# Kernel tuning notes

Hardware: AMD Instinct MI355X
Metric: run time of the kernel (lower is better)

The kernel has to match this reference:

```python
import jax, jax.numpy as jnp
import numpy as np


def _conv(x, w, b, stride=1, pad=0):
    # x: NCHW, w: OIHW (torch layout)
    y = jax.lax.conv_general_dilated(
        x, w, (stride, stride), [(pad, pad), (pad, pad)],
        dimension_numbers=('NCHW', 'OIHW', 'NCHW'))
    return y + b[None, :, None, None]


def _convT(x, w, b):
    # torch ConvTranspose2d(k=4, stride=2, padding=1); w: [Cin, Cout, 4, 4]
    wf = jnp.flip(w, (2, 3)).transpose(1, 0, 2, 3)  # -> OIHW
    y = jax.lax.conv_general_dilated(
        x, wf, (1, 1), [(2, 2), (2, 2)], lhs_dilation=(2, 2),
        dimension_numbers=('NCHW', 'OIHW', 'NCHW'))
    return y + b[None, :, None, None]


def _quantize(z, embed):
    # z: [B,H,W,D], embed: [D,K]  (eval-mode _Quantize: no EMA update)
    f = z.reshape(-1, z.shape[-1])
    dist = (f * f).sum(1, keepdims=True) - 2.0 * (f @ embed) + (embed * embed).sum(0, keepdims=True)
    ind = jnp.argmin(dist, axis=1)
    q = embed.T[ind].reshape(z.shape)
    diff = jnp.mean((jax.lax.stop_gradient(q) - z) ** 2)[None]
    q = z + jax.lax.stop_gradient(q - z)  # straight-through
    return q, diff, ind.reshape(z.shape[:-1])


def setup_inputs() -> dict:
    key = jax.random.key(0)
    ks = jax.random.split(key, 22)
    s = 0.02
    r = lambda k, sh, sc=s: jax.random.normal(k, sh, jnp.float32) * sc
    z = lambda sh: jnp.zeros(sh, jnp.float32)
    return {
        'x': jax.random.normal(ks[0], (16, 3, 256, 256), jnp.float32),
        # encoder_bottom: two stride-2 4x4 convs, 3->128->128 (256->64)
        'wb1': r(ks[1], (128, 3, 4, 4)), 'bb1': z(128),
        'wb2': r(ks[2], (128, 128, 4, 4)), 'bb2': z(128),
        # encoder_top: one stride-2 4x4 conv, 128->128 (64->32)
        'wt1': r(ks[3], (128, 128, 4, 4)), 'bt1': z(128),
        # quantize_conv_t: 1x1, 128->64
        'wqt': r(ks[4], (64, 128, 1, 1)), 'bqt': z(64),
        'embed_t': jax.random.normal(ks[5], (64, 512), jnp.float32),
        # decoder_top: convT 64->64 (32->64)
        'wdt': r(ks[6], (64, 64, 4, 4)), 'bdt': z(64),
        # quantize_conv_b: 1x1, 192->64
        'wqb': r(ks[7], (64, 192, 1, 1)), 'bqb': z(64),
        'embed_b': jax.random.normal(ks[8], (64, 512), jnp.float32),
        # upsample_t: convT 64->64 (32->64)
        'wup': r(ks[9], (64, 64, 4, 4)), 'bup': z(64),
        # decoder_bottom: convT 128->64 (64->128), convT 64->3 (128->256)
        'wd1': r(ks[10], (128, 64, 4, 4)), 'bd1': z(64),
        'wd2': r(ks[11], (64, 3, 4, 4)), 'bd2': z(3),
    }


def reference(x, wb1, bb1, wb2, bb2, wt1, bt1, wqt, bqt, embed_t,
              wdt, bdt, wqb, bqb, embed_b, wup, bup, wd1, bd1, wd2, bd2):
    # ----- encode -----
    enc_b = jax.nn.relu(_conv(x, wb1, bb1, stride=2, pad=1))          # [B,128,128,128]
    enc_b = jax.nn.relu(_conv(enc_b, wb2, bb2, stride=2, pad=1))      # [B,128,64,64]
    enc_t = jax.nn.relu(_conv(enc_b, wt1, bt1, stride=2, pad=1))      # [B,128,32,32]

    qt = _conv(enc_t, wqt, bqt).transpose(0, 2, 3, 1)                 # [B,32,32,64]
    quant_t, diff_t, id_t = _quantize(qt, embed_t)
    quant_t = quant_t.transpose(0, 3, 1, 2)                           # [B,64,32,32]

    dec_t = _convT(quant_t, wdt, bdt)                                 # [B,64,64,64]
    enc_cat = jnp.concatenate([dec_t, enc_b], axis=1)                 # [B,192,64,64]

    qb = _conv(enc_cat, wqb, bqb).transpose(0, 2, 3, 1)               # [B,64,64,64]
    quant_b, diff_b, id_b = _quantize(qb, embed_b)
    quant_b = quant_b.transpose(0, 3, 1, 2)                           # [B,64,64,64]

    loss_commit = diff_t + diff_b                                     # [1]

    # ----- decode -----
    up_t = _convT(quant_t, wup, bup)                                  # [B,64,64,64]
    quant = jnp.concatenate([up_t, quant_b], axis=1)                  # [B,128,64,64]
    h = jax.nn.relu(_convT(quant, wd1, bd1))                          # [B,64,128,128]
    x_hat = _convT(h, wd2, bd2)                                       # [B,3,256,256]

    return x_hat, quant_t, quant_b, loss_commit, id_t, id_b
```

## Files before the change

### kernel.cpp

```cpp
#include <hip/hip_runtime.h>

#define TPB 256

typedef __attribute__((ext_vector_type(4))) float f32x4;
typedef __attribute__((ext_vector_type(8))) short bf16x8;

__global__ void wtrans_kernel(const float* __restrict__ src, float* __restrict__ dst,
                              int CIN, int COUT, int taps, int iohw) {
    int idx = blockIdx.x * TPB + threadIdx.x;
    int tot = CIN * COUT * taps;
    if (idx >= tot) return;
    int co = idx % COUT;
    int ci = (idx / COUT) % CIN;
    int tap = idx / (COUT * CIN);
    float v = iohw ? src[(ci * COUT + co) * taps + tap]
                   : src[(co * CIN + ci) * taps + tap];
    dst[idx] = v;
}

__device__ __forceinline__ unsigned bf16_rne(float v) {
    unsigned u = __float_as_uint(v);
    return (u + 0x7FFFu + ((u >> 16) & 1u)) >> 16;
}

__global__ void wtrans_bf16_kernel(const float* __restrict__ src, short* __restrict__ dst,
                                   int CIN, int COUT, int taps, int iohw, int PL) {
    int idx = blockIdx.x * TPB + threadIdx.x;
    int tot = CIN * COUT * taps;
    if (idx >= tot) return;
    int ci = idx % CIN;
    int co = (idx / CIN) % COUT;
    int tap = idx / (CIN * COUT);
    float v = iohw ? src[(ci * COUT + co) * taps + tap]
                   : src[(co * CIN + ci) * taps + tap];
    unsigned h = bf16_rne(v);
    float rem = v - __uint_as_float(h << 16);
    unsigned l = bf16_rne(rem);
    dst[idx] = (short)h;
    dst[idx + PL] = (short)l;
}

__global__ void wtrans_wd2_kernel(const float* __restrict__ src, short* __restrict__ dst) {
    int idx = blockIdx.x * TPB + threadIdx.x;
    if (idx >= 16384) return;
    int ci  = idx & 63;
    int co  = (idx >> 6) & 15;
    int tap = (idx >> 10) & 3;
    int cls = idx >> 12;
    int py = cls >> 1, px = cls & 1;
    int jj = tap >> 1, ii = tap & 1;
    int ky = (1 - py) + 2 * jj;
    int kx = (1 - px) + 2 * ii;
    float v = (co < 3) ? src[(ci * 3 + co) * 16 + ky * 4 + kx] : 0.f;
    dst[idx] = (short)bf16_rne(v);
}

__global__ void etrans_kernel(const float* __restrict__ et, const float* __restrict__ eb,
                              short* __restrict__ ETt, short* __restrict__ ETb) {
    int idx = blockIdx.x * TPB + threadIdx.x;
    if (idx >= 65536) return;
    const float* src = (idx < 32768) ? et : eb;
    short* dst = (idx < 32768) ? ETt : ETb;
    int i = idx & 32767;
    int k = i & 63;
    int n = i >> 6;
    float v = src[k * 512 + n];
    unsigned h = bf16_rne(v);
    float rem = v - __uint_as_float(h << 16);
    dst[i] = (short)h;
    dst[i + 32768] = (short)bf16_rne(rem);
}

__device__ __forceinline__ void cvt_split2(float a, float b, unsigned& hw, unsigned& lw) {
    unsigned ha = bf16_rne(a), hb = bf16_rne(b);
    float ra = a - __uint_as_float(ha << 16);
    float rb = b - __uint_as_float(hb << 16);
    hw = ha | (hb << 16);
    lw = bf16_rne(ra) | (bf16_rne(rb) << 16);
}
__device__ __forceinline__ unsigned cvt_pk(float a, float b) {
    return bf16_rne(a) | (bf16_rne(b) << 16);
}

template<int MODE, int CIN, int COUT, int SPLIT, int RELU,
         int IH, int IW, int OH, int OW, int R>
__global__ __launch_bounds__(256) void mfma_conv(
    const float* __restrict__ in, const short* __restrict__ Wb,
    const float* __restrict__ bias, float* __restrict__ outp) {
    constexpr int TAPS = (MODE == 0) ? 16 : 4;
    constexpr int CW = (MODE == 0) ? OW : OW / 2;
    constexpr int CH = (MODE == 0) ? OH : OH / 2;
    constexpr int NCH = CIN / 32;
    constexpr int MTc = (COUT == 128) ? 4 : 2;
    constexpr long PL = (long)TAPS * COUT * CIN;

    __shared__ short Ah[128 * 40];
    __shared__ short Al[SPLIT ? 128 * 40 : 8];
    __shared__ short Bh[COUT * 40];
    __shared__ short Bl[SPLIT ? COUT * 40 : 8];

    int bx = blockIdx.x;
    int ry = 0, rx = 0;
    if (MODE == 1) { int c = bx & 3; ry = c >> 1; rx = c & 1; bx >>= 2; }
    const int y0 = (bx % (CH / R)) * R;
    const int n  = bx / (CH / R);

    const int tid = threadIdx.x;
    const int p  = tid >> 1;
    const int ak = (tid & 1) * 16;
    const int rr = p / CW, xx = p % CW;
    constexpr int BPT = (COUT * 32) / 256;
    constexpr int TPRB = 32 / BPT;
    const int bco = tid / TPRB;
    const int bk  = (tid % TPRB) * BPT;
    const int lane = tid & 63, wv = tid >> 6;
    const int quad = lane >> 4, l16 = lane & 15;
    const int mbase = (COUT == 128) ? (wv & 1) * 64 : wv * 32;
    const int nbase = (COUT == 128) ? (wv >> 1) * 64 : 0;

    f32x4 acc[MTc][4];
#pragma unroll
    for (int mt = 0; mt < MTc; ++mt)
#pragma unroll
        for (int nt = 0; nt < 4; ++nt) acc[mt][nt] = f32x4{0.f, 0.f, 0.f, 0.f};

#pragma unroll 1
    for (int tap = 0; tap < TAPS; ++tap) {
        int iy, ix, wt;
        if (MODE == 0) {
            int ky = tap >> 2, kx = tap & 3;
            iy = 2 * (y0 + rr) - 1 + ky;
            ix = 2 * xx - 1 + kx;
            wt = tap;
        } else {
            int jj = tap >> 1, ii = tap & 1;
            iy = (y0 + rr) + ry - jj;
            ix = xx + rx - ii;
            wt = ((1 - ry) + 2 * jj) * 4 + ((1 - rx) + 2 * ii);
        }
        const bool av = (iy >= 0) && (iy < IH) && (ix >= 0) && (ix < IW);
        const long abase = ((long)(n * IH + iy) * IW + ix) * CIN + ak;
        const short* wrh = Wb + ((long)wt * COUT + bco) * CIN + bk;

#pragma unroll 1
        for (int cb = 0; cb < NCH; ++cb) {
            __syncthreads();
            float4 f[4];
            if (av) {
                const float* sp = in + abase + cb * 32;
#pragma unroll
                for (int i = 0; i < 4; ++i) f[i] = *(const float4*)(sp + 4 * i);
            } else {
#pragma unroll
                for (int i = 0; i < 4; ++i) { f[i].x = 0.f; f[i].y = 0.f; f[i].z = 0.f; f[i].w = 0.f; }
            }
            if constexpr (SPLIT) {
                unsigned hw[8], lw[8];
#pragma unroll
                for (int i = 0; i < 4; ++i) {
                    cvt_split2(f[i].x, f[i].y, hw[2 * i], lw[2 * i]);
                    cvt_split2(f[i].z, f[i].w, hw[2 * i + 1], lw[2 * i + 1]);
                }
                *(uint4*)&Ah[p * 40 + ak]     = make_uint4(hw[0], hw[1], hw[2], hw[3]);
                *(uint4*)&Ah[p * 40 + ak + 8] = make_uint4(hw[4], hw[5], hw[6], hw[7]);
                *(uint4*)&Al[p * 40 + ak]     = make_uint4(lw[0], lw[1], lw[2], lw[3]);
                *(uint4*)&Al[p * 40 + ak + 8] = make_uint4(lw[4], lw[5], lw[6], lw[7]);
            } else {
                unsigned hw[8];
#pragma unroll
                for (int i = 0; i < 4; ++i) {
                    hw[2 * i]     = cvt_pk(f[i].x, f[i].y);
                    hw[2 * i + 1] = cvt_pk(f[i].z, f[i].w);
                }
                *(uint4*)&Ah[p * 40 + ak]     = make_uint4(hw[0], hw[1], hw[2], hw[3]);
                *(uint4*)&Ah[p * 40 + ak + 8] = make_uint4(hw[4], hw[5], hw[6], hw[7]);
            }
#pragma unroll
            for (int i = 0; i < BPT / 8; ++i) {
                *(uint4*)&Bh[bco * 40 + bk + 8 * i] = *(const uint4*)(wrh + cb * 32 + 8 * i);
                if constexpr (SPLIT)
                    *(uint4*)&Bl[bco * 40 + bk + 8 * i] = *(const uint4*)(wrh + PL + cb * 32 + 8 * i);
            }
            __syncthreads();
            bf16x8 ahf[MTc], alf[SPLIT ? MTc : 1];
#pragma unroll
            for (int mt = 0; mt < MTc; ++mt) {
                ahf[mt] = *(const bf16x8*)&Ah[(mbase + mt * 16 + l16) * 40 + quad * 8];
                if constexpr (SPLIT)
                    alf[mt] = *(const bf16x8*)&Al[(mbase + mt * 16 + l16) * 40 + quad * 8];
            }
#pragma unroll
            for (int nt = 0; nt < 4; ++nt) {
                bf16x8 bhf = *(const bf16x8*)&Bh[(nbase + nt * 16 + l16) * 40 + quad * 8];
#pragma unroll
                for (int mt = 0; mt < MTc; ++mt)
                    acc[mt][nt] = __builtin_amdgcn_mfma_f32_16x16x32_bf16(ahf[mt], bhf, acc[mt][nt], 0, 0, 0);
                if constexpr (SPLIT) {
                    bf16x8 blf = *(const bf16x8*)&Bl[(nbase + nt * 16 + l16) * 40 + quad * 8];
#pragma unroll
                    for (int mt = 0; mt < MTc; ++mt) {
                        acc[mt][nt] = __builtin_amdgcn_mfma_f32_16x16x32_bf16(alf[mt], bhf, acc[mt][nt], 0, 0, 0);
                        acc[mt][nt] = __builtin_amdgcn_mfma_f32_16x16x32_bf16(ahf[mt], blf, acc[mt][nt], 0, 0, 0);
                    }
                }
            }
        }
    }
#pragma unroll
    for (int mt = 0; mt < MTc; ++mt)
#pragma unroll
        for (int nt = 0; nt < 4; ++nt) {
            int co = nbase + nt * 16 + l16;
            float bv = bias[co];
#pragma unroll
            for (int r = 0; r < 4; ++r) {
                int pl = mbase + mt * 16 + quad * 4 + r;
                int rr2 = pl / CW, x2 = pl % CW;
                int oy, ox;
                if (MODE == 0) { oy = y0 + rr2; ox = x2; }
                else           { oy = 2 * (y0 + rr2) + ry; ox = 2 * x2 + rx; }
                float vv = acc[mt][nt][r] + bv;
                if (RELU) vv = fmaxf(vv, 0.f);
                outp[((long)(n * OH + oy) * OW + ox) * COUT + co] = vv;
            }
        }
}

__global__ __launch_bounds__(256) void convt_final_mfma(
    const float* __restrict__ h, const short* __restrict__ Wc,
    const float* __restrict__ bias, float* __restrict__ out) {
    const int HW = 128;
    __shared__ short HB[3 * 130 * 72];
    __shared__ float Sout[6 * 260];

    const int tid = threadIdx.x;
    const int y = blockIdx.x & 127;
    const int n = blockIdx.x >> 7;
    const int lane = tid & 63, wv = tid >> 6;
    const int quad = lane >> 4, l16 = lane & 15;

    for (int u = tid; u < 780; u += TPB) {
        int row = u >> 1, half = u & 1;
        int hr = row / 130, xc = row % 130;
        int hy = y - 1 + hr, hx = xc - 1;
        unsigned ww[16];
        bool ok = (hy >= 0 && hy < HW && hx >= 0 && hx < HW);
        const float* sp = h + ((long)(n * HW + hy) * HW + hx) * 64 + half * 32;
#pragma unroll
        for (int i = 0; i < 16; ++i) {
            float a = 0.f, b = 0.f;
            if (ok) { float2 p2 = *(const float2*)(sp + 2 * i); a = p2.x; b = p2.y; }
            ww[i] = cvt_pk(a, b);
        }
        short* dp = &HB[row * 72 + half * 32];
#pragma unroll
        for (int i = 0; i < 4; ++i)
            *(uint4*)(dp + 8 * i) = make_uint4(ww[4 * i], ww[4 * i + 1], ww[4 * i + 2], ww[4 * i + 3]);
    }
    __syncthreads();

#pragma unroll 1
    for (int cls = 0; cls < 4; ++cls) {
        const int py = cls >> 1, px = cls & 1;
        bf16x8 Bf[4][2];
#pragma unroll
        for (int tap = 0; tap < 4; ++tap)
#pragma unroll
            for (int cb = 0; cb < 2; ++cb)
                Bf[tap][cb] = *(const bf16x8*)&Wc[((cls * 4 + tap) * 16 + l16) * 64 + cb * 32 + quad * 8];

        f32x4 acc2[2] = { f32x4{0.f,0.f,0.f,0.f}, f32x4{0.f,0.f,0.f,0.f} };
#pragma unroll
        for (int mt = 0; mt < 2; ++mt) {
            const int xp0 = wv * 32 + mt * 16;
#pragma unroll
            for (int tap = 0; tap < 4; ++tap) {
                const int jj = tap >> 1, ii = tap & 1;
                const int hr = py - jj + 1;
                const int rbase = (hr * 130 + xp0 + l16 + px - ii + 1) * 72;
#pragma unroll
                for (int cb = 0; cb < 2; ++cb) {
                    bf16x8 Af = *(const bf16x8*)&HB[rbase + cb * 32 + quad * 8];
                    acc2[mt] = __builtin_amdgcn_mfma_f32_16x16x32_bf16(Af, Bf[tap][cb], acc2[mt], 0, 0, 0);
                }
            }
        }
        if (l16 < 3) {
#pragma unroll
            for (int mt = 0; mt < 2; ++mt)
#pragma unroll
                for (int r = 0; r < 4; ++r) {
                    int xp = wv * 32 + mt * 16 + quad * 4 + r;
                    Sout[(py * 3 + l16) * 260 + 2 * xp + px] = acc2[mt][r];
                }
        }
    }
    __syncthreads();

    for (int u = tid; u < 384; u += TPB) {
        int idx = u * 4;
        int rowi = idx >> 8;
        int xq   = idx & 255;
        int py = rowi / 3, co = rowi % 3;
        float bv = bias[co];
        float4 v = *(const float4*)&Sout[rowi * 260 + xq];
        v.x += bv; v.y += bv; v.z += bv; v.w += bv;
        *(float4*)&out[(((long)(n * 3 + co) * 256) + 2 * y + py) * 256 + xq] = v;
    }
}

__global__ __launch_bounds__(256) void conv1_kernel(
    const float* __restrict__ x, const float* __restrict__ Wt,
    const float* __restrict__ bias, float* __restrict__ out) {
    const int IH = 256, IW = 256, OH = 128, OW = 128, BM = 64;
    int bx = blockIdx.x;
    int sx = bx & 1;
    int oy = (bx >> 1) & 127;
    int n  = bx >> 8;
    int ox0 = sx * BM;
    __shared__ float Bs[16 * 3 * 128];
    __shared__ float Ts[3 * 4 * 132];
    int tid = threadIdx.x;
    for (int i = tid; i < 6144 / 4; i += TPB)
        ((float4*)Bs)[i] = ((const float4*)Wt)[i];
    int iy0 = 2 * oy - 1;
    for (int idx = tid; idx < 3 * 4 * 130; idx += TPB) {
        int ci = idx / 520; int r = idx % 520;
        int ky = r / 130;   int xx = r % 130;
        int iy = iy0 + ky;  int ix = 2 * ox0 - 1 + xx;
        float v = 0.f;
        if (iy >= 0 && iy < IH && ix >= 0 && ix < IW)
            v = x[((n * 3 + ci) * IH + iy) * IW + ix];
        Ts[(ci * 4 + ky) * 132 + xx] = v;
    }
    __syncthreads();
    int cog = tid & 31, pxg = tid >> 5;
    int co0 = cog * 4, px0 = pxg * 8;
    float acc[8][4];
#pragma unroll
    for (int i = 0; i < 8; ++i)
#pragma unroll
        for (int j = 0; j < 4; ++j) acc[i][j] = 0.f;
#pragma unroll 1
    for (int ky = 0; ky < 4; ++ky)
#pragma unroll 1
        for (int kx = 0; kx < 4; ++kx)
#pragma unroll
            for (int ci = 0; ci < 3; ++ci) {
                float4 b = *(const float4*)&Bs[((ky * 4 + kx) * 3 + ci) * 128 + co0];
                const float* trow = &Ts[(ci * 4 + ky) * 132 + kx];
#pragma unroll
                for (int q = 0; q < 8; ++q) {
                    float a = trow[2 * (px0 + q)];
                    acc[q][0] = fmaf(a, b.x, acc[q][0]);
                    acc[q][1] = fmaf(a, b.y, acc[q][1]);
                    acc[q][2] = fmaf(a, b.z, acc[q][2]);
                    acc[q][3] = fmaf(a, b.w, acc[q][3]);
                }
            }
    float4 bb = *(const float4*)&bias[co0];
#pragma unroll
    for (int q = 0; q < 8; ++q) {
        int ox = ox0 + px0 + q;
        float4 v;
        v.x = fmaxf(acc[q][0] + bb.x, 0.f);
        v.y = fmaxf(acc[q][1] + bb.y, 0.f);
        v.z = fmaxf(acc[q][2] + bb.z, 0.f);
        v.w = fmaxf(acc[q][3] + bb.w, 0.f);
        *(float4*)&out[(((long)n * OH + oy) * OW + ox) * 128 + co0] = v;
    }
}

template<int MODE, int CIN, int COUT, int BM, int RELU, int IH, int IW, int OH, int OW>
__global__ __launch_bounds__(256) void conv_gemm(
    const float* __restrict__ in, const float* __restrict__ Wt,
    const float* __restrict__ bias, float* __restrict__ out) {
    constexpr int CHUNK  = 64;
    constexpr int NCH    = CIN / CHUNK;
    constexpr int CO_PER = (COUT == 128) ? 4 : 2;
    constexpr int PX_PER = BM / 8;
    constexpr int TAPS   = (MODE == 0) ? 16 : (MODE == 1 ? 4 : 1);
    __shared__ float As[CHUNK * BM];
    __shared__ float Bs[CHUNK * COUT];
    const int tid = threadIdx.x;
    const int bx  = blockIdx.x;
    int n, oy, ox0 = 0, par = 0;
    if (MODE == 1) {
        par = bx & 1;
        oy  = (bx >> 1) % OH;
        n   = bx / (2 * OH);
    } else {
        constexpr int SPR = OW / BM;
        int s = bx % SPR;
        oy = (bx / SPR) % OH;
        n  = bx / (SPR * OH);
        ox0 = s * BM;
    }
    const int cog = tid & 31;
    const int pxg = tid >> 5;
    const int co0 = cog * CO_PER, px0 = pxg * PX_PER;
    float acc[PX_PER][CO_PER];
#pragma unroll
    for (int q = 0; q < PX_PER; ++q)
#pragma unroll
        for (int j = 0; j < CO_PER; ++j) acc[q][j] = 0.f;
    constexpr int TPX  = 256 / BM;
    constexpr int CIPT = CHUNK / TPX;
    const int spx  = tid / TPX;
    const int sci0 = (tid % TPX) * CIPT;
    const int py   = oy & 1;

#pragma unroll 1
    for (int tap = 0; tap < TAPS; ++tap) {
        int iy, twi, sx;
        if (MODE == 0) {
            int ky = tap >> 2, kx = tap & 3;
            iy  = 2 * oy - 1 + ky;
            sx  = 2 * (ox0 + spx) - 1 + kx;
            twi = tap;
        } else if (MODE == 1) {
            int jj = tap >> 1, ii = tap & 1;
            iy  = ((oy + 1) >> 1) - jj;
            sx  = spx + par - ii;
            twi = ((1 - py) + 2 * jj) * 4 + ((1 - par) + 2 * ii);
        } else {
            iy = oy; sx = ox0 + spx; twi = 0;
        }
        const bool pxv = (iy >= 0) && (iy < IH) && (sx >= 0) && (sx < IW);
        const float* srcp = in + (((long)n * IH + iy) * IW + sx) * CIN + sci0;
#pragma unroll 1
        for (int cb = 0; cb < NCH; ++cb) {
            __syncthreads();
            float4 tmp[CIPT / 4];
#pragma unroll
            for (int t4 = 0; t4 < CIPT / 4; ++t4) {
                if (pxv) tmp[t4] = *(const float4*)(srcp + cb * CHUNK + 4 * t4);
                else { tmp[t4].x = 0.f; tmp[t4].y = 0.f; tmp[t4].z = 0.f; tmp[t4].w = 0.f; }
            }
#pragma unroll
            for (int t4 = 0; t4 < CIPT / 4; ++t4) {
                As[(sci0 + 4 * t4 + 0) * BM + spx] = tmp[t4].x;
                As[(sci0 + 4 * t4 + 1) * BM + spx] = tmp[t4].y;
                As[(sci0 + 4 * t4 + 2) * BM + spx] = tmp[t4].z;
                As[(sci0 + 4 * t4 + 3) * BM + spx] = tmp[t4].w;
            }
            {
                const float4* wsrc = (const float4*)(Wt + ((long)twi * CIN + cb * CHUNK) * COUT);
#pragma unroll
                for (int t4 = 0; t4 < (CHUNK * COUT) / 1024; ++t4)
                    ((float4*)Bs)[tid + 256 * t4] = wsrc[tid + 256 * t4];
            }
            __syncthreads();
#pragma unroll 4
            for (int k = 0; k < CHUNK; ++k) {
                float a[PX_PER];
#pragma unroll
                for (int t4 = 0; t4 < PX_PER / 4; ++t4)
                    *(float4*)&a[4 * t4] = *(const float4*)&As[k * BM + px0 + 4 * t4];
                if constexpr (CO_PER == 4) {
                    float4 b = *(const float4*)&Bs[k * COUT + co0];
#pragma unroll
                    for (int q = 0; q < PX_PER; ++q) {
                        acc[q][0] = fmaf(a[q], b.x, acc[q][0]);
                        acc[q][1] = fmaf(a[q], b.y, acc[q][1]);
                        acc[q][2] = fmaf(a[q], b.z, acc[q][2]);
                        acc[q][3] = fmaf(a[q], b.w, acc[q][3]);
                    }
                } else {
                    float2 b = *(const float2*)&Bs[k * COUT + co0];
#pragma unroll
                    for (int q = 0; q < PX_PER; ++q) {
                        acc[q][0] = fmaf(a[q], b.x, acc[q][0]);
                        acc[q][1] = fmaf(a[q], b.y, acc[q][1]);
                    }
                }
            }
        }
    }
    float bv[CO_PER];
#pragma unroll
    for (int j = 0; j < CO_PER; ++j) bv[j] = bias[co0 + j];
#pragma unroll
    for (int q = 0; q < PX_PER; ++q) {
        int ox = (MODE == 1) ? (par + 2 * (px0 + q)) : (ox0 + px0 + q);
        float* op = out + (((long)n * OH + oy) * OW + ox) * COUT + co0;
        if constexpr (CO_PER == 4) {
            float4 v;
            v.x = acc[q][0] + bv[0]; v.y = acc[q][1] + bv[1];
            v.z = acc[q][2] + bv[2]; v.w = acc[q][3] + bv[3];
            if (RELU) { v.x = fmaxf(v.x, 0.f); v.y = fmaxf(v.y, 0.f);
                        v.z = fmaxf(v.z, 0.f); v.w = fmaxf(v.w, 0.f); }
            *(float4*)op = v;
        } else {
            float2 v;
            v.x = acc[q][0] + bv[0]; v.y = acc[q][1] + bv[1];
            if (RELU) { v.x = fmaxf(v.x, 0.f); v.y = fmaxf(v.y, 0.f); }
            *(float2*)op = v;
        }
    }
}

__global__ void enorm_kernel(const float* __restrict__ et, const float* __restrict__ eb,
                             float* __restrict__ nt, float* __restrict__ nb) {
    int k = blockIdx.x * TPB + threadIdx.x;
    if (k >= 1024) return;
    const float* e = (k < 512) ? et : eb;
    float* o = (k < 512) ? nt : nb;
    int kk = k & 511;
    float s = 0.f;
#pragma unroll 8
    for (int d = 0; d < 64; ++d) { float v = e[d * 512 + kk]; s = fmaf(v, v, s); }
    o[kk] = s;
}

__global__ __launch_bounds__(256) void quantize_mfma(
    const float* __restrict__ f, const short* __restrict__ ET,
    const float* __restrict__ embed, const float* __restrict__ enorm,
    float* __restrict__ qn, float* __restrict__ qc, float* __restrict__ ido,
    float* __restrict__ dsum, int M, int HW) {
    __shared__ short Fh[64 * 72];
    __shared__ short Fl[64 * 72];
    __shared__ float S[64 * 65];
    __shared__ int   KI[64];
    __shared__ float wsum[4];

    const int tid = threadIdx.x;
    const int lane = tid & 63, wv = tid >> 6;
    const int quad = lane >> 4, l16 = lane & 15;
    const int R0 = blockIdx.x * 64;

    {
        int row = tid >> 2;
        int k0 = (tid & 3) * 16;
        const float* sp = f + (long)(R0 + row) * 64 + k0;
        unsigned hw[8], lw[8];
#pragma unroll
        for (int i = 0; i < 4; ++i) {
            float4 p = *(const float4*)(sp + 4 * i);
            cvt_split2(p.x, p.y, hw[2 * i], lw[2 * i]);
            cvt_split2(p.z, p.w, hw[2 * i + 1], lw[2 * i + 1]);
        }
        short* dh = &Fh[row * 72 + k0];
        short* dl = &Fl[row * 72 + k0];
        *(uint4*)(dh)     = make_uint4(hw[0], hw[1], hw[2], hw[3]);
        *(uint4*)(dh + 8) = make_uint4(hw[4], hw[5], hw[6], hw[7]);
        *(uint4*)(dl)     = make_uint4(lw[0], lw[1], lw[2], lw[3]);
        *(uint4*)(dl + 8) = make_uint4(lw[4], lw[5], lw[6], lw[7]);
    }
    __syncthreads();

    const int arow = (wv * 16 + l16) * 72;
    bf16x8 Ah0 = *(const bf16x8*)&Fh[arow + quad * 8];
    bf16x8 Ah1 = *(const bf16x8*)&Fh[arow + 32 + quad * 8];
    bf16x8 Al0 = *(const bf16x8*)&Fl[arow + quad * 8];
    bf16x8 Al1 = *(const bf16x8*)&Fl[arow + 32 + quad * 8];

    float bestv[4];
    int   besti[4];
#pragma unroll
    for (int r = 0; r < 4; ++r) { bestv[r] = 3.4e38f; besti[r] = 0; }

    const short* ETlo = ET + 32768;
#pragma unroll 2
    for (int j = 0; j < 32; ++j) {
        const int nb = (j * 16 + l16) * 64 + quad * 8;
        bf16x8 Bh0 = *(const bf16x8*)(ET + nb);
        bf16x8 Bh1 = *(const bf16x8*)(ET + nb + 32);
        bf16x8 Bl0 = *(const bf16x8*)(ETlo + nb);
        bf16x8 Bl1 = *(const bf16x8*)(ETlo + nb + 32);
        f32x4 acc = f32x4{0.f, 0.f, 0.f, 0.f};
        acc = __builtin_amdgcn_mfma_f32_16x16x32_bf16(Ah0, Bh0, acc, 0, 0, 0);
        acc = __builtin_amdgcn_mfma_f32_16x16x32_bf16(Ah1, Bh1, acc, 0, 0, 0);
        acc = __builtin_amdgcn_mfma_f32_16x16x32_bf16(Al0, Bh0, acc, 0, 0, 0);
        acc = __builtin_amdgcn_mfma_f32_16x16x32_bf16(Al1, Bh1, acc, 0, 0, 0);
        acc = __builtin_amdgcn_mfma_f32_16x16x32_bf16(Ah0, Bl0, acc, 0, 0, 0);
        acc = __builtin_amdgcn_mfma_f32_16x16x32_bf16(Ah1, Bl1, acc, 0, 0, 0);
        float en = enorm[j * 16 + l16];
        int   ni = j * 16 + l16;
#pragma unroll
        for (int r = 0; r < 4; ++r) {
            float s = fmaf(-2.f, acc[r], en);
            if (s < bestv[r]) { bestv[r] = s; besti[r] = ni; }
        }
    }
#pragma unroll
    for (int m = 1; m < 16; m <<= 1) {
#pragma unroll
        for (int r = 0; r < 4; ++r) {
            float ov = __shfl_xor(bestv[r], m);
            int   oi = __shfl_xor(besti[r], m);
            if (ov < bestv[r] || (ov == bestv[r] && oi < besti[r])) {
                bestv[r] = ov; besti[r] = oi;
            }
        }
    }
    if (l16 == 0) {
#pragma unroll
        for (int r = 0; r < 4; ++r) KI[wv * 16 + quad * 4 + r] = besti[r];
    }
    __syncthreads();

    float ddacc = 0.f;
#pragma unroll 1
    for (int r16 = 0; r16 < 16; ++r16) {
        int row = wv * 16 + r16;
        int k = KI[row];
        float ev = embed[lane * 512 + k];
        float fv = f[(long)(R0 + row) * 64 + lane];
        qn[(long)(R0 + row) * 64 + lane] = ev;
        S[row * 65 + lane] = ev;
        float dq = ev - fv;
        ddacc = fmaf(dq, dq, ddacc);
        if (lane == 0) ido[R0 + row] = (float)k;
    }
#pragma unroll
    for (int off = 1; off < 64; off <<= 1) ddacc += __shfl_xor(ddacc, off);
    if (lane == 0) wsum[wv] = ddacc;
    __syncthreads();
    if (tid == 0)
        atomicAdd(dsum, wsum[0] + wsum[1] + wsum[2] + wsum[3]);

    int nn = R0 / HW;
    int rem0 = R0 - nn * HW;
    int px = tid & 63;
    int cg = tid >> 6;
#pragma unroll
    for (int it = 0; it < 16; ++it) {
        int c = cg + 4 * it;
        qc[((long)nn * 64 + c) * HW + rem0 + px] = S[px * 65 + c];
    }
}

__global__ void concat_kernel(const float* __restrict__ a, const float* __restrict__ b,
                              float* __restrict__ o, int ca, int cb, int M) {
    int fpr = (ca + cb) >> 2;
    int idx = blockIdx.x * TPB + threadIdx.x;
    if (idx >= M * fpr) return;
    int row = idx / fpr;
    int c4  = (idx - row * fpr) * 4;
    float4 v;
    if (c4 < ca) v = *(const float4*)(a + (long)row * ca + c4);
    else         v = *(const float4*)(b + (long)row * cb + (c4 - ca));
    *(float4*)(o + (long)row * (ca + cb) + c4) = v;
}

__global__ void loss_kernel(const float* __restrict__ sums, float* __restrict__ out) {
    out[0] = sums[0] * (1.f / (16384.f * 64.f)) + sums[1] * (1.f / (65536.f * 64.f));
}

extern "C" void kernel_launch(void* const* d_in, const int* in_sizes, int n_in,
                              void* d_out, int out_size, void* d_ws, size_t ws_size,
                              hipStream_t stream) {
    const float* x   = (const float*)d_in[0];
    const float* wb1 = (const float*)d_in[1];  const float* bb1 = (const float*)d_in[2];
    const float* wb2 = (const float*)d_in[3];  const float* bb2 = (const float*)d_in[4];
    const float* wt1 = (const float*)d_in[5];  const float* bt1 = (const float*)d_in[6];
    const float* wqt = (const float*)d_in[7];  const float* bqt = (const float*)d_in[8];
    const float* embed_t = (const float*)d_in[9];
    const float* wdt = (const float*)d_in[10]; const float* bdt = (const float*)d_in[11];
    const float* wqb = (const float*)d_in[12]; const float* bqb = (const float*)d_in[13];
    const float* embed_b = (const float*)d_in[14];
    const float* wup = (const float*)d_in[15]; const float* bup = (const float*)d_in[16];
    const float* wd1 = (const float*)d_in[17]; const float* bd1 = (const float*)d_in[18];
    const float* wd2 = (const float*)d_in[19]; const float* bd2 = (const float*)d_in[20];
    float* out = (float*)d_out;
    float* ws  = (float*)d_ws;

    float* O_XHAT = out;
    float* O_QT   = out + 3145728;
    float* O_QB   = out + 4194304;
    float* O_LOSS = out + 8388608;
    float* O_IDT  = out + 8388609;
    float* O_IDB  = out + 8404993;

    float* W_WB1 = ws + 0;
    short* WB_WD2 = (short*)(ws + 16384);
    short* ET_T  = (short*)(ws + 32768);
    short* ET_B  = (short*)(ws + 65536);
    float* W_WQT = ws + 532480;
    float* W_WDT = ws + 540672;
    float* W_WQB = ws + 606208;
    float* EN_T  = ws + 818176;
    float* EN_B  = ws + 818688;
    float* SUMS  = ws + 819200;
    float* T1    = ws + 1048576;
    const long BIG = 9437184;
    float* T0   = ws + BIG;
    float* T2   = ws + BIG;
    float* QT   = ws + BIG + 2097152;
    float* QTN  = ws + BIG + 3145728;
    float* DECT = ws + BIG + 4194304;
    float* ECAT = ws + BIG + 8388608;
    float* QB   = ws + BIG + 20971520;
    float* QBN  = ws + BIG + 25165824;
    float* UPT  = ws + BIG + 4194304;
    float* QCAT = ws + BIG + 8388608;
    float* HBUF = ws + BIG + 16777216;
    short* WB_BF2 = (short*)(ws + 42991616);
    short* WB_BT1 = (short*)(ws + 43253760);
    short* WB_BD1 = (short*)(ws + 43515904);
    short* WB_BUP = (short*)(ws + 43646976);

    auto wt_launch = [&](const float* src, float* dst, int cin, int cout, int taps, int iohw) {
        int tot = cin * cout * taps;
        wtrans_kernel<<<(tot + TPB - 1) / TPB, TPB, 0, stream>>>(src, dst, cin, cout, taps, iohw);
    };
    auto wtb_launch = [&](const float* src, short* dst, int cin, int cout, int taps, int iohw) {
        int tot = cin * cout * taps;
        wtrans_bf16_kernel<<<(tot + TPB - 1) / TPB, TPB, 0, stream>>>(src, dst, cin, cout, taps, iohw, tot);
    };
    wt_launch(wb1, W_WB1, 3, 128, 16, 0);
    wt_launch(wqt, W_WQT, 128, 64, 1, 0);
    wt_launch(wdt, W_WDT, 64, 64, 16, 1);
    wt_launch(wqb, W_WQB, 192, 64, 1, 0);
    wtrans_wd2_kernel<<<64, TPB, 0, stream>>>(wd2, WB_WD2);
    wtb_launch(wb2, WB_BF2, 128, 128, 16, 0);
    wtb_launch(wt1, WB_BT1, 128, 128, 16, 0);
    wtb_launch(wd1, WB_BD1, 128, 64, 16, 1);
    wtb_launch(wup, WB_BUP, 64, 64, 16, 1);
    enorm_kernel<<<4, TPB, 0, stream>>>(embed_t, embed_b, EN_T, EN_B);
    etrans_kernel<<<256, TPB, 0, stream>>>(embed_t, embed_b, ET_T, ET_B);
    hipError_t e0 = hipMemsetAsync((void*)SUMS, 0, 2 * sizeof(float), stream);
    (void)e0;

    conv1_kernel<<<4096, TPB, 0, stream>>>(x, W_WB1, bb1, T0);
    mfma_conv<0, 128, 128, 1, 1, 128, 128, 64, 64, 2><<<512, TPB, 0, stream>>>(T0, WB_BF2, bb2, T1);
    mfma_conv<0, 128, 128, 1, 1, 64, 64, 32, 32, 4><<<128, TPB, 0, stream>>>(T1, WB_BT1, bt1, T2);
    conv_gemm<2, 128, 64, 32, 0, 32, 32, 32, 32><<<512, TPB, 0, stream>>>(T2, W_WQT, bqt, QT);
    quantize_mfma<<<256, TPB, 0, stream>>>(QT, ET_T, embed_t, EN_T, QTN, O_QT, O_IDT, SUMS,
                                           16384, 1024);
    conv_gemm<1, 64, 64, 32, 0, 32, 32, 64, 64><<<2048, TPB, 0, stream>>>(QTN, W_WDT, bdt, DECT);
    concat_kernel<<<12288, TPB, 0, stream>>>(DECT, T1, ECAT, 64, 128, 65536);
    conv_gemm<2, 192, 64, 64, 0, 64, 64, 64, 64><<<1024, TPB, 0, stream>>>(ECAT, W_WQB, bqb, QB);
    quantize_mfma<<<1024, TPB, 0, stream>>>(QB, ET_B, embed_b, EN_B, QBN, O_QB, O_IDB, SUMS + 1,
                                            65536, 4096);
    mfma_conv<1, 64, 64, 0, 0, 32, 32, 64, 64, 4><<<512, TPB, 0, stream>>>(QTN, WB_BUP, bup, UPT);
    concat_kernel<<<8192, TPB, 0, stream>>>(UPT, QBN, QCAT, 64, 64, 65536);
    mfma_conv<1, 128, 64, 0, 1, 64, 64, 128, 128, 2><<<2048, TPB, 0, stream>>>(QCAT, WB_BD1, bd1, HBUF);
    convt_final_mfma<<<2048, TPB, 0, stream>>>(HBUF, WB_WD2, bd2, O_XHAT);
    loss_kernel<<<1, 1, 0, stream>>>(SUMS, O_LOSS);

    (void)in_sizes; (void)n_in; (void)out_size; (void)ws_size;
}
```

Measured before the change: 802.1 us.

## Store intermediate activations as bf16 hi/lo planes to cut conversion and traffic

Producers now write activations already split into bf16 high and low planes, or single bf16 for the decoder path, instead of fp32. Consumers (mfma_conv, convt_final) load bf16 directly without per-tile fp32-to-bf16 conversion. Intermediate tensor bandwidth is lower, though the split format takes the same bytes as fp32 for the split paths. The concat kernels are specialised, including a reconstruction of fp32 from the split planes. This changes buffer layouts across several stages, and T1's fp32 value is now rebuilt from two bf16 parts.

Measured after the change: 707.5 us. -11.8%, faster.

```diff
diff --git a/kernel.cpp b/kernel.cpp
--- a/kernel.cpp
+++ b/kernel.cpp
@@ -83,16 +83,19 @@
 }
 
 template<int MODE, int CIN, int COUT, int SPLIT, int RELU,
-         int IH, int IW, int OH, int OW, int R>
+         int IH, int IW, int OH, int OW, int R, int INBF, int OUTB>
 __global__ __launch_bounds__(256) void mfma_conv(
-    const float* __restrict__ in, const short* __restrict__ Wb,
-    const float* __restrict__ bias, float* __restrict__ outp) {
+    const void* __restrict__ inv, const short* __restrict__ Wb,
+    const float* __restrict__ bias, float* __restrict__ outp,
+    short* __restrict__ outb) {
     constexpr int TAPS = (MODE == 0) ? 16 : 4;
     constexpr int CW = (MODE == 0) ? OW : OW / 2;
     constexpr int CH = (MODE == 0) ? OH : OH / 2;
     constexpr int NCH = CIN / 32;
     constexpr int MTc = (COUT == 128) ? 4 : 2;
     constexpr long PL = (long)TAPS * COUT * CIN;
+    constexpr long APL_IN  = 16L * IH * IW * CIN;
+    constexpr long APL_OUT = 16L * OH * OW * COUT;
 
     __shared__ short Ah[128 * 40];
     __shared__ short Al[SPLIT ? 128 * 40 : 8];
@@ -145,35 +148,51 @@
 #pragma unroll 1
         for (int cb = 0; cb < NCH; ++cb) {
             __syncthreads();
-            float4 f[4];
-            if (av) {
-                const float* sp = in + abase + cb * 32;
-#pragma unroll
-                for (int i = 0; i < 4; ++i) f[i] = *(const float4*)(sp + 4 * i);
+            if constexpr (INBF) {
+                const short* sb = (const short*)inv + abase + cb * 32;
+                uint4 h0, h1;
+                if (av) { h0 = *(const uint4*)sb; h1 = *(const uint4*)(sb + 8); }
+                else { h0 = make_uint4(0,0,0,0); h1 = h0; }
+                *(uint4*)&Ah[p * 40 + ak]     = h0;
+                *(uint4*)&Ah[p * 40 + ak + 8] = h1;
+                if constexpr (SPLIT) {
+                    uint4 l0, l1;
+                    if (av) { l0 = *(const uint4*)(sb + APL_IN); l1 = *(const uint4*)(sb + APL_IN + 8); }
+                    else { l0 = make_uint4(0,0,0,0); l1 = l0; }
+                    *(uint4*)&Al[p * 40 + ak]     = l0;
+                    *(uint4*)&Al[p * 40 + ak + 8] = l1;
+                }
             } else {
-#pragma unroll
-                for (int i = 0; i < 4; ++i) { f[i].x = 0.f; f[i].y = 0.f; f[i].z = 0.f; f[i].w = 0.f; }
-            }
-            if constexpr (SPLIT) {
-                unsigned hw[8], lw[8];
-#pragma unroll
-                for (int i = 0; i < 4; ++i) {
-                    cvt_split2(f[i].x, f[i].y, hw[2 * i], lw[2 * i]);
-                    cvt_split2(f[i].z, f[i].w, hw[2 * i + 1], lw[2 * i + 1]);
-                }
-                *(uint4*)&Ah[p * 40 + ak]     = make_uint4(hw[0], hw[1], hw[2], hw[3]);
-                *(uint4*)&Ah[p * 40 + ak + 8] = make_uint4(hw[4], hw[5], hw[6], hw[7]);
-                *(uint4*)&Al[p * 40 + ak]     = make_uint4(lw[0], lw[1], lw[2], lw[3]);
-                *(uint4*)&Al[p * 40 + ak + 8] = make_uint4(lw[4], lw[5], lw[6], lw[7]);
-            } else {
-                unsigned hw[8];
-#pragma unroll
-                for (int i = 0; i < 4; ++i) {
-                    hw[2 * i]     = cvt_pk(f[i].x, f[i].y);
-                    hw[2 * i + 1] = cvt_pk(f[i].z, f[i].w);
-                }
-                *(uint4*)&Ah[p * 40 + ak]     = make_uint4(hw[0], hw[1], hw[2], hw[3]);
-                *(uint4*)&Ah[p * 40 + ak + 8] = make_uint4(hw[4], hw[5], hw[6], hw[7]);
+                const float* sp = (const float*)inv + abase + cb * 32;
+                float4 f[4];
+                if (av) {
+#pragma unroll
+                    for (int i = 0; i < 4; ++i) f[i] = *(const float4*)(sp + 4 * i);
+                } else {
+#pragma unroll
+                    for (int i = 0; i < 4; ++i) { f[i].x = 0.f; f[i].y = 0.f; f[i].z = 0.f; f[i].w = 0.f; }
+                }
+                if constexpr (SPLIT) {
+                    unsigned hw[8], lw[8];
+#pragma unroll
+                    for (int i = 0; i < 4; ++i) {
+                        cvt_split2(f[i].x, f[i].y, hw[2 * i], lw[2 * i]);
+                        cvt_split2(f[i].z, f[i].w, hw[2 * i + 1], lw[2 * i + 1]);
+                    }
+                    *(uint4*)&Ah[p * 40 + ak]     = make_uint4(hw[0], hw[1], hw[2], hw[3]);
+                    *(uint4*)&Ah[p * 40 + ak + 8] = make_uint4(hw[4], hw[5], hw[6], hw[7]);
+                    *(uint4*)&Al[p * 40 + ak]     = make_uint4(lw[0], lw[1], lw[2], lw[3]);
+                    *(uint4*)&Al[p * 40 + ak + 8] = make_uint4(lw[4], lw[5], lw[6], lw[7]);
+                } else {
+                    unsigned hw[8];
+#pragma unroll
+                    for (int i = 0; i < 4; ++i) {
+                        hw[2 * i]     = cvt_pk(f[i].x, f[i].y);
+                        hw[2 * i + 1] = cvt_pk(f[i].z, f[i].w);
+                    }
+                    *(uint4*)&Ah[p * 40 + ak]     = make_uint4(hw[0], hw[1], hw[2], hw[3]);
+                    *(uint4*)&Ah[p * 40 + ak + 8] = make_uint4(hw[4], hw[5], hw[6], hw[7]);
+                }
             }
 #pragma unroll
             for (int i = 0; i < BPT / 8; ++i) {
@@ -221,13 +240,20 @@
                 else           { oy = 2 * (y0 + rr2) + ry; ox = 2 * x2 + rx; }
                 float vv = acc[mt][nt][r] + bv;
                 if (RELU) vv = fmaxf(vv, 0.f);
-                outp[((long)(n * OH + oy) * OW + ox) * COUT + co] = vv;
+                long oidx = ((long)(n * OH + oy) * OW + ox) * COUT + co;
+                if constexpr (OUTB == 0 || OUTB == 1) outp[oidx] = vv;
+                if constexpr (OUTB == 1 || OUTB == 3) {
+                    unsigned hh = bf16_rne(vv);
+                    outb[oidx] = (short)hh;
+                    outb[oidx + APL_OUT] = (short)bf16_rne(vv - __uint_as_float(hh << 16));
+                }
+                if constexpr (OUTB == 2) outb[oidx] = (short)bf16_rne(vv);
             }
         }
 }
 
 __global__ __launch_bounds__(256) void convt_final_mfma(
-    const float* __restrict__ h, const short* __restrict__ Wc,
+    const short* __restrict__ h, const short* __restrict__ Wc,
     const float* __restrict__ bias, float* __restrict__ out) {
     const int HW = 128;
     __shared__ short HB[3 * 130 * 72];
@@ -243,19 +269,18 @@
         int row = u >> 1, half = u & 1;
         int hr = row / 130, xc = row % 130;
         int hy = y - 1 + hr, hx = xc - 1;
-        unsigned ww[16];
         bool ok = (hy >= 0 && hy < HW && hx >= 0 && hx < HW);
-        const float* sp = h + ((long)(n * HW + hy) * HW + hx) * 64 + half * 32;
-#pragma unroll
-        for (int i = 0; i < 16; ++i) {
-            float a = 0.f, b = 0.f;
-            if (ok) { float2 p2 = *(const float2*)(sp + 2 * i); a = p2.x; b = p2.y; }
-            ww[i] = cvt_pk(a, b);
+        const short* sp = h + ((long)(n * HW + hy) * HW + hx) * 64 + half * 32;
+        uint4 a0, a1, a2, a3;
+        if (ok) {
+            a0 = *(const uint4*)sp;       a1 = *(const uint4*)(sp + 8);
+            a2 = *(const uint4*)(sp + 16); a3 = *(const uint4*)(sp + 24);
+        } else {
+            a0 = make_uint4(0,0,0,0); a1 = a0; a2 = a0; a3 = a0;
         }
         short* dp = &HB[row * 72 + half * 32];
-#pragma unroll
-        for (int i = 0; i < 4; ++i)
-            *(uint4*)(dp + 8 * i) = make_uint4(ww[4 * i], ww[4 * i + 1], ww[4 * i + 2], ww[4 * i + 3]);
+        *(uint4*)dp = a0; *(uint4*)(dp + 8) = a1;
+        *(uint4*)(dp + 16) = a2; *(uint4*)(dp + 24) = a3;
     }
     __syncthreads();
 
@@ -311,8 +336,9 @@
 
 __global__ __launch_bounds__(256) void conv1_kernel(
     const float* __restrict__ x, const float* __restrict__ Wt,
-    const float* __restrict__ bias, float* __restrict__ out) {
+    const float* __restrict__ bias, short* __restrict__ outb) {
     const int IH = 256, IW = 256, OH = 128, OW = 128, BM = 64;
+    const long APL0 = 16L * 128 * 128 * 128;
     int bx = blockIdx.x;
     int sx = bx & 1;
     int oy = (bx >> 1) & 127;
@@ -362,12 +388,16 @@
 #pragma unroll
     for (int q = 0; q < 8; ++q) {
         int ox = ox0 + px0 + q;
-        float4 v;
-        v.x = fmaxf(acc[q][0] + bb.x, 0.f);
-        v.y = fmaxf(acc[q][1] + bb.y, 0.f);
-        v.z = fmaxf(acc[q][2] + bb.z, 0.f);
-        v.w = fmaxf(acc[q][3] + bb.w, 0.f);
-        *(float4*)&out[(((long)n * OH + oy) * OW + ox) * 128 + co0] = v;
+        float v0 = fmaxf(acc[q][0] + bb.x, 0.f);
+        float v1 = fmaxf(acc[q][1] + bb.y, 0.f);
+        float v2 = fmaxf(acc[q][2] + bb.z, 0.f);
+        float v3 = fmaxf(acc[q][3] + bb.w, 0.f);
+        unsigned h0, l0, h1, l1;
+        cvt_split2(v0, v1, h0, l0);
+        cvt_split2(v2, v3, h1, l1);
+        long pix = ((long)n * OH + oy) * OW + ox;
+        *(uint2*)&outb[pix * 128 + co0]        = make_uint2(h0, h1);
+        *(uint2*)&outb[APL0 + pix * 128 + co0] = make_uint2(l0, l1);
     }
 }
 
@@ -631,17 +661,37 @@
     }
 }
 
-__global__ void concat_kernel(const float* __restrict__ a, const float* __restrict__ b,
-                              float* __restrict__ o, int ca, int cb, int M) {
-    int fpr = (ca + cb) >> 2;
+__global__ void concat_rec_kernel(const float* __restrict__ a, const short* __restrict__ bh,
+                                  float* __restrict__ o, int M) {
+    const long PLB = 8388608L;
     int idx = blockIdx.x * TPB + threadIdx.x;
-    if (idx >= M * fpr) return;
-    int row = idx / fpr;
-    int c4  = (idx - row * fpr) * 4;
+    if (idx >= M * 48) return;
+    int row = idx / 48;
+    int c4  = (idx - row * 48) * 4;
     float4 v;
-    if (c4 < ca) v = *(const float4*)(a + (long)row * ca + c4);
-    else         v = *(const float4*)(b + (long)row * cb + (c4 - ca));
-    *(float4*)(o + (long)row * (ca + cb) + c4) = v;
+    if (c4 < 64) v = *(const float4*)(a + (long)row * 64 + c4);
+    else {
+        int cc = c4 - 64;
+        uint2 h = *(const uint2*)(bh + (long)row * 128 + cc);
+        uint2 l = *(const uint2*)(bh + PLB + (long)row * 128 + cc);
+        v.x = __uint_as_float(h.x << 16)        + __uint_as_float(l.x << 16);
+        v.y = __uint_as_float(h.x & 0xFFFF0000u) + __uint_as_float(l.x & 0xFFFF0000u);
+        v.z = __uint_as_float(h.y << 16)        + __uint_as_float(l.y << 16);
+        v.w = __uint_as_float(h.y & 0xFFFF0000u) + __uint_as_float(l.y & 0xFFFF0000u);
+    }
+    *(float4*)(o + (long)row * 192 + c4) = v;
+}
+
+__global__ void concat_bf16_kernel(const float* __restrict__ a, const float* __restrict__ b,
+                                   short* __restrict__ o, int M) {
+    int idx = blockIdx.x * TPB + threadIdx.x;
+    if (idx >= M * 32) return;
+    int row = idx / 32;
+    int c4  = (idx - row * 32) * 4;
+    float4 v;
+    if (c4 < 64) v = *(const float4*)(a + (long)row * 64 + c4);
+    else         v = *(const float4*)(b + (long)row * 64 + (c4 - 64));
+    *(uint2*)(o + (long)row * 128 + c4) = make_uint2(cvt_pk(v.x, v.y), cvt_pk(v.z, v.w));
 }
 
 __global__ void loss_kernel(const float* __restrict__ sums, float* __restrict__ out) {
@@ -683,9 +733,9 @@
     float* EN_T  = ws + 818176;
     float* EN_B  = ws + 818688;
     float* SUMS  = ws + 819200;
-    float* T1    = ws + 1048576;
+    short* T1B  = (short*)(ws + 1048576);
     const long BIG = 9437184;
-    float* T0   = ws + BIG;
+    short* T0B  = (short*)(ws + BIG);
     float* T2   = ws + BIG;
     float* QT   = ws + BIG + 2097152;
     float* QTN  = ws + BIG + 3145728;
@@ -694,8 +744,8 @@
     float* QB   = ws + BIG + 20971520;
     float* QBN  = ws + BIG + 25165824;
     float* UPT  = ws + BIG + 4194304;
-    float* QCAT = ws + BIG + 8388608;
-    float* HBUF = ws + BIG + 16777216;
+    short* QCATB = (short*)(ws + BIG + 8388608);
+    short* HBUFB = (short*)(ws + BIG + 16777216);
     short* WB_BF2 = (short*)(ws + 42991616);
     short* WB_BT1 = (short*)(ws + 43253760);
     short* WB_BD1 = (short*)(ws + 43515904);
@@ -723,21 +773,25 @@
     hipError_t e0 = hipMemsetAsync((void*)SUMS, 0, 2 * sizeof(float), stream);
     (void)e0;
 
-    conv1_kernel<<<4096, TPB, 0, stream>>>(x, W_WB1, bb1, T0);
-    mfma_conv<0, 128, 128, 1, 1, 128, 128, 64, 64, 2><<<512, TPB, 0, stream>>>(T0, WB_BF2, bb2, T1);
-    mfma_conv<0, 128, 128, 1, 1, 64, 64, 32, 32, 4><<<128, TPB, 0, stream>>>(T1, WB_BT1, bt1, T2);
+    conv1_kernel<<<4096, TPB, 0, stream>>>(x, W_WB1, bb1, T0B);
+    mfma_conv<0, 128, 128, 1, 1, 128, 128, 64, 64, 2, 1, 3>
+        <<<512, TPB, 0, stream>>>(T0B, WB_BF2, bb2, nullptr, T1B);
+    mfma_conv<0, 128, 128, 1, 1, 64, 64, 32, 32, 4, 1, 0>
+        <<<128, TPB, 0, stream>>>(T1B, WB_BT1, bt1, T2, nullptr);
     conv_gemm<2, 128, 64, 32, 0, 32, 32, 32, 32><<<512, TPB, 0, stream>>>(T2, W_WQT, bqt, QT);
     quantize_mfma<<<256, TPB, 0, stream>>>(QT, ET_T, embed_t, EN_T, QTN, O_QT, O_IDT, SUMS,
                                            16384, 1024);
     conv_gemm<1, 64, 64, 32, 0, 32, 32, 64, 64><<<2048, TPB, 0, stream>>>(QTN, W_WDT, bdt, DECT);
-    concat_kernel<<<12288, TPB, 0, stream>>>(DECT, T1, ECAT, 64, 128, 65536);
+    concat_rec_kernel<<<12288, TPB, 0, stream>>>(DECT, T1B, ECAT, 65536);
     conv_gemm<2, 192, 64, 64, 0, 64, 64, 64, 64><<<1024, TPB, 0, stream>>>(ECAT, W_WQB, bqb, QB);
     quantize_mfma<<<1024, TPB, 0, stream>>>(QB, ET_B, embed_b, EN_B, QBN, O_QB, O_IDB, SUMS + 1,
                                             65536, 4096);
-    mfma_conv<1, 64, 64, 0, 0, 32, 32, 64, 64, 4><<<512, TPB, 0, stream>>>(QTN, WB_BUP, bup, UPT);
-    concat_kernel<<<8192, TPB, 0, stream>>>(UPT, QBN, QCAT, 64, 64, 65536);
-    mfma_conv<1, 128, 64, 0, 1, 64, 64, 128, 128, 2><<<2048, TPB, 0, stream>>>(QCAT, WB_BD1, bd1, HBUF);
-    convt_final_mfma<<<2048, TPB, 0, stream>>>(HBUF, WB_WD2, bd2, O_XHAT);
+    mfma_conv<1, 64, 64, 0, 0, 32, 32, 64, 64, 4, 0, 0>
+        <<<512, TPB, 0, stream>>>(QTN, WB_BUP, bup, UPT, nullptr);
+    concat_bf16_kernel<<<8192, TPB, 0, stream>>>(UPT, QBN, QCATB, 65536);
+    mfma_conv<1, 128, 64, 0, 1, 64, 64, 128, 128, 2, 1, 2>
+        <<<2048, TPB, 0, stream>>>(QCATB, WB_BD1, bd1, nullptr, HBUFB);
+    convt_final_mfma<<<2048, TPB, 0, stream>>>(HBUFB, WB_WD2, bd2, O_XHAT);
     loss_kernel<<<1, 1, 0, stream>>>(SUMS, O_LOSS);
 
     (void)in_sizes; (void)n_in; (void)out_size; (void)ws_size;
```
